# Optimization experiments

Measured on AMD Instinct MI355X. Metric: run time of the kernel, lower is better.

## Reference

```python
import jax, jax.numpy as jnp
import numpy as np

EMBED_DIM = 256
NUM_HEADS = 8
NB = 8          # number of scenes (batches)
LQ = 256        # queries per scene
LS = 4096       # source points per scene
LN_EPS = 1e-5


def setup_inputs() -> dict:
    key = jax.random.key(0)
    ks = jax.random.split(key, 8)
    d = EMBED_DIM
    n_q, n_s = NB * LQ, NB * LS
    w_scale = d ** -0.5  # xavier-ish
    return {
        "source": jax.random.normal(ks[0], (n_s, d), jnp.float32),
        "query": jax.random.normal(ks[1], (n_q, d), jnp.float32),
        "source_pe": 0.1 * jax.random.normal(ks[2], (n_s, d), jnp.float32),
        "query_pe": 0.1 * jax.random.normal(ks[3], (n_q, d), jnp.float32),
        "in_proj_w": w_scale * jax.random.normal(ks[4], (3 * d, d), jnp.float32),
        "in_proj_b": jnp.zeros((3 * d,), jnp.float32),
        "out_w": w_scale * jax.random.normal(ks[5], (d, d), jnp.float32),
        "out_b": jnp.zeros((d,), jnp.float32),
        "ln_w": jnp.ones((d,), jnp.float32),
        "ln_b": jnp.zeros((d,), jnp.float32),
        # sorted equal-size segments: token i belongs to scene i // L
        "source_batch": (jnp.arange(n_s, dtype=jnp.int32) // LS).astype(jnp.int32),
        "query_batch": (jnp.arange(n_q, dtype=jnp.int32) // LQ).astype(jnp.int32),
        "B": NB,
    }


def reference(source, query, source_pe, query_pe, in_proj_w, in_proj_b,
              out_w, out_b, ln_w, ln_b, source_batch, query_batch, B):
    d = source.shape[-1]
    H = NUM_HEADS
    hd = d // H
    Lq = query.shape[0] // B
    Ls = source.shape[0] // B

    # batch ids are sorted equal segments -> per-scene gather == reshape
    q_in = (query + query_pe).reshape(B, Lq, d)   # q with pos embed
    k_in = (source + source_pe).reshape(B, Ls, d) # k with pos embed
    v_in = source.reshape(B, Ls, d)               # v without pos embed

    Wq, Wk, Wv = jnp.split(in_proj_w, 3, axis=0)
    bq, bk, bv = jnp.split(in_proj_b, 3)

    q = (q_in @ Wq.T + bq).reshape(B, Lq, H, hd)
    k = (k_in @ Wk.T + bk).reshape(B, Ls, H, hd)
    v = (v_in @ Wv.T + bv).reshape(B, Ls, H, hd)

    scores = jnp.einsum('bqhd,bkhd->bhqk', q, k) * (hd ** -0.5)
    attn = jax.nn.softmax(scores, axis=-1)
    o = jnp.einsum('bhqk,bkhd->bqhd', attn, v).reshape(B, Lq, d)
    o = o @ out_w.T + out_b

    # residual (dropout is identity at p=0) + LayerNorm
    res = o + query.reshape(B, Lq, d)
    mu = jnp.mean(res, axis=-1, keepdims=True)
    var = jnp.var(res, axis=-1, keepdims=True)
    y = (res - mu) * jax.lax.rsqrt(var + LN_EPS) * ln_w + ln_b
    return y.reshape(-1, d)
```

## Files before the change

### kernel.cpp

```cpp
#include <hip/hip_runtime.h>
#include <hip/hip_bf16.h>

typedef __bf16 bf16;
typedef __bf16 bf16x4 __attribute__((ext_vector_type(4)));
typedef __bf16 bf16x8 __attribute__((ext_vector_type(8)));
typedef float f32x4 __attribute__((ext_vector_type(4)));

#define D 256
#define NHEAD 8
#define HD 32
#define NB_ 8
#define LQ_ 256
#define LS_ 4096
#define MQ (NB_ * LQ_)
#define MS (NB_ * LS_)

#define QSCALE 0.25500527f

__global__ __launch_bounds__(256) void prep(
    const float* __restrict__ source, const float* __restrict__ source_pe,
    const float* __restrict__ query, const float* __restrict__ query_pe,
    const float* __restrict__ w_in, const float* __restrict__ w_out,
    bf16* __restrict__ SPb, bf16* __restrict__ QPb, bf16* __restrict__ Wb)
{
    const int NS4 = MS * D / 4;
    const int NQ4 = MQ * D / 4;
    const int NW4 = (768 * 256 + 256 * 256) / 4;
    const int total = NS4 + NQ4 + NW4;
    for (int i = blockIdx.x * 256 + threadIdx.x; i < total; i += gridDim.x * 256) {
        if (i < NS4) {
            const float4 s = ((const float4*)source)[i];
            const float4 p = ((const float4*)source_pe)[i];
            bf16x4 osp;
            osp[0] = (bf16)(s.x + p.x); osp[1] = (bf16)(s.y + p.y);
            osp[2] = (bf16)(s.z + p.z); osp[3] = (bf16)(s.w + p.w);
            ((bf16x4*)SPb)[i] = osp;
        } else if (i < NS4 + NQ4) {
            const int j = i - NS4;
            const float4 s = ((const float4*)query)[j];
            const float4 p = ((const float4*)query_pe)[j];
            bf16x4 o;
            o[0] = (bf16)(s.x + p.x); o[1] = (bf16)(s.y + p.y);
            o[2] = (bf16)(s.z + p.z); o[3] = (bf16)(s.w + p.w);
            ((bf16x4*)QPb)[j] = o;
        } else {
            const int j = i - NS4 - NQ4;
            const float4 v = (j < 49152) ? ((const float4*)w_in)[j]
                                         : ((const float4*)w_out)[j - 49152];
            bf16x4 o;
            o[0] = (bf16)v.x; o[1] = (bf16)v.y; o[2] = (bf16)v.z; o[3] = (bf16)v.w;
            ((bf16x4*)Wb)[j] = o;
        }
    }
}

__global__ __launch_bounds__(256, 4) void gemm_proj(
    const bf16* __restrict__ SPb, const float* __restrict__ srcf,
    const bf16* __restrict__ QPb, const bf16* __restrict__ Wb,
    const float* __restrict__ in_proj_b,
    bf16* __restrict__ Kt, bf16* __restrict__ Vt2, bf16* __restrict__ Qb)
{
    __shared__ __align__(16) bf16 smem[2][128][72];
    bf16 (*As)[72] = smem[0];
    bf16 (*Bs)[72] = smem[1];
    const int tid = threadIdx.x, lane = tid & 63, wid = tid >> 6;
    const int wm = wid >> 1, wn = wid & 1;
    const int g = lane >> 4, q15 = lane & 15;
    const int id = blockIdx.x;

    const bf16* A; const bf16* W; const float* bias; bf16* out;
    int omode, mblk, nblk;
    if (id < 512) {
        A = SPb; W = Wb + 256 * D; bias = in_proj_b + 256; out = Kt;
        mblk = id >> 1; nblk = id & 1; omode = 1;
    } else if (id < 1024) {
        A = nullptr; W = Wb + 512 * D; bias = in_proj_b + 512; out = Vt2;
        mblk = (id - 512) >> 1; nblk = id & 1; omode = 2;
    } else {
        A = QPb; W = Wb; bias = in_proj_b; out = Qb;
        mblk = (id - 1024) >> 1; nblk = id & 1; omode = 0;
    }

    f32x4 acc[4][4];
    #pragma unroll
    for (int i = 0; i < 4; ++i)
        #pragma unroll
        for (int j = 0; j < 4; ++j) acc[i][j] = (f32x4){0.f, 0.f, 0.f, 0.f};

    const size_t arow0 = (size_t)mblk * 128;
    const int brow0 = nblk * 128;

    for (int kk = 0; kk < 4; ++kk) {
        const int d0 = kk * 64;
        if (omode == 2) {
            #pragma unroll
            for (int i = 0; i < 8; ++i) {
                const int idx = i * 256 + tid;
                const int r = idx >> 4, c = (idx & 15) * 4;
                const float4 v = *(const float4*)&srcf[(arow0 + r) * D + d0 + c];
                bf16x4 o;
                o[0] = (bf16)v.x; o[1] = (bf16)v.y; o[2] = (bf16)v.z; o[3] = (bf16)v.w;
                *(bf16x4*)&As[r][c] = o;
            }
            #pragma unroll
            for (int i = 0; i < 4; ++i) {
                const int idx = i * 256 + tid;
                const int r = idx >> 3, c = (idx & 7) * 8;
                *(bf16x8*)&Bs[r][c] = *(const bf16x8*)&W[(size_t)(brow0 + r) * D + d0 + c];
            }
        } else {
            #pragma unroll
            for (int i = 0; i < 4; ++i) {
                const int idx = i * 256 + tid;
                const int r = idx >> 3, c = (idx & 7) * 8;
                *(bf16x8*)&As[r][c] = *(const bf16x8*)&A[(arow0 + r) * D + d0 + c];
                *(bf16x8*)&Bs[r][c] = *(const bf16x8*)&W[(size_t)(brow0 + r) * D + d0 + c];
            }
        }
        __syncthreads();
        #pragma unroll
        for (int h2 = 0; h2 < 2; ++h2) {
            const int ko = h2 * 32 + g * 8;
            bf16x8 af[4], bfr[4];
            #pragma unroll
            for (int i = 0; i < 4; ++i)
                af[i] = *(const bf16x8*)&As[wm * 64 + i * 16 + q15][ko];
            #pragma unroll
            for (int j = 0; j < 4; ++j)
                bfr[j] = *(const bf16x8*)&Bs[wn * 64 + j * 16 + q15][ko];
            #pragma unroll
            for (int i = 0; i < 4; ++i)
                #pragma unroll
                for (int j = 0; j < 4; ++j)
                    acc[i][j] = __builtin_amdgcn_mfma_f32_16x16x32_bf16(
                        af[i], bfr[j], acc[i][j], 0, 0, 0);
        }
        __syncthreads();
    }

    if (omode == 0) {
        #pragma unroll
        for (int i = 0; i < 4; ++i)
            #pragma unroll
            for (int j = 0; j < 4; ++j) {
                const int n_g = nblk * 128 + wn * 64 + j * 16 + q15;
                const float b = bias[n_g];
                #pragma unroll
                for (int r = 0; r < 4; ++r) {
                    const size_t m_g = arow0 + wm * 64 + i * 16 + g * 4 + r;
                    out[m_g * D + n_g] = (bf16)((acc[i][j][r] + b) * QSCALE);
                }
            }
    } else if (omode == 1) {
        bf16* Ls = &smem[0][0][0];
        #pragma unroll
        for (int i = 0; i < 4; ++i)
            #pragma unroll
            for (int j = 0; j < 4; ++j) {
                const int n_loc = wn * 64 + j * 16 + q15;
                const int h_loc = n_loc >> 5, d = n_loc & 31;
                const int gp = d >> 3, e = d & 7;
                const float b = bias[nblk * 128 + n_loc];
                #pragma unroll
                for (int r = 0; r < 4; ++r) {
                    const int m_loc = wm * 64 + i * 16 + g * 4 + r;
                    const int c_loc = m_loc >> 6, kl = m_loc & 63;
                    const int t = ((kl >> 5) << 1) | ((kl >> 2) & 1);
                    const int q15p = ((kl >> 3) & 3) * 4 + (kl & 3);
                    Ls[(h_loc * 2 + c_loc) * 2048 + t * 512
                       + (gp * 16 + q15p) * 8 + e] = (bf16)(acc[i][j][r] + b);
                }
            }
        __syncthreads();
        const int bb = (int)(arow0 >> 12);
        const int c0 = (int)((arow0 & 4095) >> 6);
        const int h0 = (nblk * 128) >> 5;
        #pragma unroll
        for (int p = 0; p < 8; ++p) {
            const int idx = p * 2048 + tid * 8;
            const int blk = idx >> 11, within = idx & 2047;
            *(bf16x8*)&out[((size_t)(bb * 8 + h0 + (blk >> 1)) * 64
                            + c0 + (blk & 1)) * 2048 + within]
                = *(const bf16x8*)&Ls[idx];
        }
    } else {
        #pragma unroll
        for (int i = 0; i < 4; ++i)
            #pragma unroll
            for (int j = 0; j < 4; ++j) {
                const int n_g = nblk * 128 + wn * 64 + j * 16 + q15;
                const int h = n_g >> 5, d = n_g & 31;
                const int dt = d >> 4, q15p = d & 15;
                const float b = bias[n_g];
                const size_t m_g0 = arow0 + wm * 64 + i * 16 + g * 4;
                const int bb = (int)(m_g0 >> 12);
                const int c = (int)((m_g0 & 4095) >> 6);
                const int kl0 = (int)(m_g0 & 63);
                const int half = kl0 >> 5, gp = (kl0 >> 3) & 3, e0 = kl0 & 7;
                const int f = dt * 2 + half;
                bf16x4 o;
                #pragma unroll
                for (int r = 0; r < 4; ++r) o[r] = (bf16)(acc[i][j][r] + b);
                *(bf16x4*)&out[((size_t)(bb * 8 + h) * 64 + c) * 2048
                               + f * 512 + (gp * 16 + q15p) * 8 + e0] = o;
            }
    }
}

template<int S>
__global__ __launch_bounds__(256, 4) void attn_kernel(
    const bf16* __restrict__ Qb, const bf16* __restrict__ Kt,
    const bf16* __restrict__ Vt2,
    bf16* __restrict__ accp, float* __restrict__ lp)
{
    const int tid = threadIdx.x, lane = tid & 63, wid = tid >> 6;
    const int q15 = lane & 15, g = lane >> 4;
    const int bid = blockIdx.x;
    const int h = bid & 7;
    const int inner = bid >> 3;
    const int split = inner % S;
    const int tmp = inner / S;
    const int qt = tmp & 1;
    const int b = tmp >> 1;
    constexpr int CHUNKS = LS_ / S / 64;

    const int q0 = b * LQ_ + qt * 128 + wid * 32;
    const bf16x8 qfA = *(const bf16x8*)&Qb[(size_t)(q0 + q15) * D + h * HD + g * 8];
    const bf16x8 qfB = *(const bf16x8*)&Qb[(size_t)(q0 + 16 + q15) * D + h * HD + g * 8];

    const f32x4 minit = (f32x4){-8.f, -8.f, -8.f, -8.f};
    const size_t cbase = ((size_t)(b * 8 + h) * 64 + split * CHUNKS) * 2048;
    const bf16* kp = Kt + cbase + lane * 8;
    const bf16* vp = Vt2 + cbase + lane * 8;

    float lA = 0.f, lB = 0.f;
    f32x4 accA0 = (f32x4){0.f, 0.f, 0.f, 0.f};
    f32x4 accA1 = (f32x4){0.f, 0.f, 0.f, 0.f};
    f32x4 accB0 = (f32x4){0.f, 0.f, 0.f, 0.f};
    f32x4 accB1 = (f32x4){0.f, 0.f, 0.f, 0.f};

    for (int kc = 0; kc < CHUNKS; ++kc) {
        const size_t co = (size_t)kc * 2048;

        bf16x8 kf[4], vf[4];
        #pragma unroll
        for (int t = 0; t < 4; ++t) kf[t] = *(const bf16x8*)&kp[co + t * 512];
        #pragma unroll
        for (int f = 0; f < 4; ++f) vf[f] = *(const bf16x8*)&vp[co + f * 512];

        f32x4 sA[4], sB[4];
        #pragma unroll
        for (int t = 0; t < 4; ++t)
            sA[t] = __builtin_amdgcn_mfma_f32_16x16x32_bf16(kf[t], qfA, minit, 0, 0, 0);
        #pragma unroll
        for (int t = 0; t < 4; ++t)
            sB[t] = __builtin_amdgcn_mfma_f32_16x16x32_bf16(kf[t], qfB, minit, 0, 0, 0);

        bf16x8 paA0, paA1, paB0, paB1;
        #pragma unroll
        for (int r = 0; r < 4; ++r) {
            const float a0 = exp2f(sA[0][r]);
            const float a1 = exp2f(sA[1][r]);
            const float a2 = exp2f(sA[2][r]);
            const float a3 = exp2f(sA[3][r]);
            lA += (a0 + a1) + (a2 + a3);
            paA0[r] = (bf16)a0; paA0[4 + r] = (bf16)a1;
            paA1[r] = (bf16)a2; paA1[4 + r] = (bf16)a3;
            const float b0 = exp2f(sB[0][r]);
            const float b1 = exp2f(sB[1][r]);
            const float b2 = exp2f(sB[2][r]);
            const float b3 = exp2f(sB[3][r]);
            lB += (b0 + b1) + (b2 + b3);
            paB0[r] = (bf16)b0; paB0[4 + r] = (bf16)b1;
            paB1[r] = (bf16)b2; paB1[4 + r] = (bf16)b3;
        }

        accA0 = __builtin_amdgcn_mfma_f32_16x16x32_bf16(paA0, vf[0], accA0, 0, 0, 0);
        accA0 = __builtin_amdgcn_mfma_f32_16x16x32_bf16(paA1, vf[1], accA0, 0, 0, 0);
        accA1 = __builtin_amdgcn_mfma_f32_16x16x32_bf16(paA0, vf[2], accA1, 0, 0, 0);
        accA1 = __builtin_amdgcn_mfma_f32_16x16x32_bf16(paA1, vf[3], accA1, 0, 0, 0);
        accB0 = __builtin_amdgcn_mfma_f32_16x16x32_bf16(paB0, vf[0], accB0, 0, 0, 0);
        accB0 = __builtin_amdgcn_mfma_f32_16x16x32_bf16(paB1, vf[1], accB0, 0, 0, 0);
        accB1 = __builtin_amdgcn_mfma_f32_16x16x32_bf16(paB0, vf[2], accB1, 0, 0, 0);
        accB1 = __builtin_amdgcn_mfma_f32_16x16x32_bf16(paB1, vf[3], accB1, 0, 0, 0);
    }

    lA += __shfl_xor(lA, 16);
    lA += __shfl_xor(lA, 32);
    lB += __shfl_xor(lB, 16);
    lB += __shfl_xor(lB, 32);

    const int qg16 = qt * 8 + wid * 2;
    const int taskA = (b * 8 + h) * 16 + qg16;
    const size_t baseA = ((size_t)(taskA * S + split) * 64 + lane) * 8;
    const size_t baseB = ((size_t)((taskA + 1) * S + split) * 64 + lane) * 8;
    bf16x4 oA0, oA1, oB0, oB1;
    #pragma unroll
    for (int r = 0; r < 4; ++r) {
        oA0[r] = (bf16)accA0[r]; oA1[r] = (bf16)accA1[r];
        oB0[r] = (bf16)accB0[r]; oB1[r] = (bf16)accB1[r];
    }
    *(bf16x4*)&accp[baseA]     = oA0;
    *(bf16x4*)&accp[baseA + 4] = oA1;
    *(bf16x4*)&accp[baseB]     = oB0;
    *(bf16x4*)&accp[baseB + 4] = oB1;
    if (lane < 16) {
        lp[(taskA * S + split) * 16 + lane] = lA;
        lp[((taskA + 1) * S + split) * 16 + lane] = lB;
    }
}

template<int S>
__global__ __launch_bounds__(256) void attn_combine(
    const bf16* __restrict__ accp, const float* __restrict__ lp,
    bf16* __restrict__ Ob)
{
    const int tid = threadIdx.x, lane = tid & 63, wid = tid >> 6;
    const int task = blockIdx.x * 4 + wid;
    const int g = lane >> 4, q15 = lane & 15;

    f32x4 o0 = (f32x4){0.f, 0.f, 0.f, 0.f};
    f32x4 o1 = (f32x4){0.f, 0.f, 0.f, 0.f};
    float ll = 0.f;
    #pragma unroll
    for (int s = 0; s < S; ++s) {
        const size_t base = ((size_t)(task * S + s) * 64 + lane) * 8;
        const bf16x8 v = *(const bf16x8*)&accp[base];
        #pragma unroll
        for (int r = 0; r < 4; ++r) { o0[r] += (float)v[r]; o1[r] += (float)v[4 + r]; }
        if (lane < 16) ll += lp[(task * S + s) * 16 + lane];
    }

    const int b = task >> 7, h = (task >> 4) & 7, qg = task & 15;
    #pragma unroll
    for (int r = 0; r < 4; ++r) {
        const float inv = 1.f / __shfl(ll, g * 4 + r);
        const size_t row = (size_t)b * LQ_ + qg * 16 + g * 4 + r;
        Ob[row * D + h * HD + q15]      = (bf16)(o0[r] * inv);
        Ob[row * D + h * HD + 16 + q15] = (bf16)(o1[r] * inv);
    }
}

__global__ __launch_bounds__(256) void out_ln_kernel(
    const bf16* __restrict__ Ob, const bf16* __restrict__ Wout,
    const float* __restrict__ out_b, const float* __restrict__ query,
    const float* __restrict__ lnw, const float* __restrict__ lnb,
    float* __restrict__ out)
{
    __shared__ bf16 As[32][72];
    __shared__ bf16 Bs[256][72];
    __shared__ float red[2][32][2];
    const int tid = threadIdx.x, lane = tid & 63, wid = tid >> 6;
    const int wm = wid >> 1, wn = wid & 1;
    const int g = lane >> 4, q15 = lane & 15;
    const size_t row0 = (size_t)blockIdx.x * 32;

    f32x4 acc[8];
    #pragma unroll
    for (int j = 0; j < 8; ++j) acc[j] = (f32x4){0.f, 0.f, 0.f, 0.f};

    for (int kk = 0; kk < 4; ++kk) {
        const int d0 = kk * 64;
        {
            const int r = tid >> 3, c = (tid & 7) * 8;
            *(bf16x8*)&As[r][c] = *(const bf16x8*)&Ob[(row0 + r) * D + d0 + c];
        }
        #pragma unroll
        for (int i = 0; i < 8; ++i) {
            const int idx = i * 256 + tid;
            const int r = idx >> 3, c = (idx & 7) * 8;
            *(bf16x8*)&Bs[r][c] = *(const bf16x8*)&Wout[(size_t)r * D + d0 + c];
        }
        __syncthreads();
        #pragma unroll
        for (int h2 = 0; h2 < 2; ++h2) {
            const int ko = h2 * 32 + g * 8;
            const bf16x8 af = *(const bf16x8*)&As[wm * 16 + q15][ko];
            #pragma unroll
            for (int j = 0; j < 8; ++j) {
                const bf16x8 bfr = *(const bf16x8*)&Bs[wn * 128 + j * 16 + q15][ko];
                acc[j] = __builtin_amdgcn_mfma_f32_16x16x32_bf16(af, bfr, acc[j], 0, 0, 0);
            }
        }
        __syncthreads();
    }

    float bl[8], lw[8], lbv[8];
    #pragma unroll
    for (int j = 0; j < 8; ++j) {
        const int n = wn * 128 + j * 16 + q15;
        bl[j] = out_b[n]; lw[j] = lnw[n]; lbv[j] = lnb[n];
    }

    #pragma unroll
    for (int r = 0; r < 4; ++r) {
        const int rl = wm * 16 + g * 4 + r;
        const size_t m = row0 + rl;
        float s = 0.f, sq = 0.f;
        #pragma unroll
        for (int j = 0; j < 8; ++j) {
            const float v = acc[j][r] + bl[j] + query[m * D + wn * 128 + j * 16 + q15];
            acc[j][r] = v;
            s += v; sq += v * v;
        }
        s += __shfl_xor(s, 1);  sq += __shfl_xor(sq, 1);
        s += __shfl_xor(s, 2);  sq += __shfl_xor(sq, 2);
        s += __shfl_xor(s, 4);  sq += __shfl_xor(sq, 4);
        s += __shfl_xor(s, 8);  sq += __shfl_xor(sq, 8);
        if (q15 == r) {
            red[wn][rl][0] = s;
            red[wn][rl][1] = sq;
        }
    }
    __syncthreads();

    #pragma unroll
    for (int r = 0; r < 4; ++r) {
        const int rl = wm * 16 + g * 4 + r;
        const float s  = red[0][rl][0] + red[1][rl][0];
        const float sq = red[0][rl][1] + red[1][rl][1];
        const float mean = s * (1.f / 256.f);
        const float var  = sq * (1.f / 256.f) - mean * mean;
        const float inv  = rsqrtf(var + 1e-5f);
        const size_t m = row0 + rl;
        #pragma unroll
        for (int j = 0; j < 8; ++j)
            out[m * D + wn * 128 + j * 16 + q15] =
                (acc[j][r] - mean) * inv * lw[j] + lbv[j];
    }
}

extern "C" void kernel_launch(void* const* d_in, const int* in_sizes, int n_in,
                              void* d_out, int out_size, void* d_ws, size_t ws_size,
                              hipStream_t stream) {
    (void)in_sizes; (void)n_in; (void)out_size; (void)ws_size;
    const float* source    = (const float*)d_in[0];
    const float* query     = (const float*)d_in[1];
    const float* source_pe = (const float*)d_in[2];
    const float* query_pe  = (const float*)d_in[3];
    const float* in_proj_w = (const float*)d_in[4];
    const float* in_proj_b = (const float*)d_in[5];
    const float* out_w     = (const float*)d_in[6];
    const float* out_b     = (const float*)d_in[7];
    const float* ln_w      = (const float*)d_in[8];
    const float* ln_b      = (const float*)d_in[9];

    constexpr int S = 8;
    bf16* Wb   = (bf16*)d_ws;
    bf16* QPb  = Wb + 1024 * 256;
    bf16* Qb   = QPb + (size_t)MQ * D;
    bf16* Kt   = Qb + (size_t)MQ * D;
    bf16* Vt2  = Kt + (size_t)MS * D;
    bf16* SPb  = Vt2 + (size_t)MS * D;
    bf16* Ob   = SPb + (size_t)MS * D;
    bf16* accp = Ob + (size_t)MQ * D;
    float* lp  = (float*)(accp + (size_t)1024 * S * 64 * 8);
    float* outp = (float*)d_out;

    prep<<<dim3(2048), dim3(256), 0, stream>>>(
        source, source_pe, query, query_pe, in_proj_w, out_w,
        SPb, QPb, Wb);
    gemm_proj<<<dim3(1056), dim3(256), 0, stream>>>(
        SPb, source, QPb, Wb, in_proj_b, Kt, Vt2, Qb);
    attn_kernel<S><<<dim3(1024), dim3(256), 0, stream>>>(Qb, Kt, Vt2, accp, lp);
    attn_combine<S><<<dim3(256), dim3(256), 0, stream>>>(accp, lp, Ob);
    out_ln_kernel<<<dim3(64), dim3(256), 0, stream>>>(
        Ob, Wb + 768 * 256, out_b, query, ln_w, ln_b, outp);
}
```

Measured before the change: 81.01 us.

## Fuse pos-embed add into projection GEMM and split-K combine into out-proj LN

Removes the prep pass that materialized bf16 source+pe and query+pe buffers; the projection GEMM now loads fp32 inputs, adds the positional embedding and casts to bf16 while filling shared memory. A small kernel now only casts the weights. The separate attention combine kernel is folded into the output-projection/LayerNorm kernel, which reduces the split partials straight into a full-row shared tile, so the Ob buffer is no longer written or read. This cuts global traffic and launches, at the cost of the K-projection blocks reading two fp32 arrays, and the out-proj kernel running only 64 blocks, which now also do the combine work.

```diff
diff --git a/kernel.cpp b/kernel.cpp
--- a/kernel.cpp
+++ b/kernel.cpp
@@ -17,47 +17,24 @@
 
 #define QSCALE 0.25500527f
 
-__global__ __launch_bounds__(256) void prep(
+__global__ __launch_bounds__(256) void wcast(
+    const float* __restrict__ w_in, const float* __restrict__ w_out,
+    bf16* __restrict__ wb)
+{
+    const int idx = blockIdx.x * 256 + threadIdx.x;
+    const int n_in4 = (768 * 256) / 4;
+    float4 v;
+    if (idx < n_in4) v = ((const float4*)w_in)[idx];
+    else             v = ((const float4*)w_out)[idx - n_in4];
+    bf16x4 o;
+    o[0] = (bf16)v.x; o[1] = (bf16)v.y; o[2] = (bf16)v.z; o[3] = (bf16)v.w;
+    *(bf16x4*)&wb[(size_t)idx * 4] = o;
+}
+
+__global__ __launch_bounds__(256, 4) void gemm_proj(
     const float* __restrict__ source, const float* __restrict__ source_pe,
     const float* __restrict__ query, const float* __restrict__ query_pe,
-    const float* __restrict__ w_in, const float* __restrict__ w_out,
-    bf16* __restrict__ SPb, bf16* __restrict__ QPb, bf16* __restrict__ Wb)
-{
-    const int NS4 = MS * D / 4;
-    const int NQ4 = MQ * D / 4;
-    const int NW4 = (768 * 256 + 256 * 256) / 4;
-    const int total = NS4 + NQ4 + NW4;
-    for (int i = blockIdx.x * 256 + threadIdx.x; i < total; i += gridDim.x * 256) {
-        if (i < NS4) {
-            const float4 s = ((const float4*)source)[i];
-            const float4 p = ((const float4*)source_pe)[i];
-            bf16x4 osp;
-            osp[0] = (bf16)(s.x + p.x); osp[1] = (bf16)(s.y + p.y);
-            osp[2] = (bf16)(s.z + p.z); osp[3] = (bf16)(s.w + p.w);
-            ((bf16x4*)SPb)[i] = osp;
-        } else if (i < NS4 + NQ4) {
-            const int j = i - NS4;
-            const float4 s = ((const float4*)query)[j];
-            const float4 p = ((const float4*)query_pe)[j];
-            bf16x4 o;
-            o[0] = (bf16)(s.x + p.x); o[1] = (bf16)(s.y + p.y);
-            o[2] = (bf16)(s.z + p.z); o[3] = (bf16)(s.w + p.w);
-            ((bf16x4*)QPb)[j] = o;
-        } else {
-            const int j = i - NS4 - NQ4;
-            const float4 v = (j < 49152) ? ((const float4*)w_in)[j]
-                                         : ((const float4*)w_out)[j - 49152];
-            bf16x4 o;
-            o[0] = (bf16)v.x; o[1] = (bf16)v.y; o[2] = (bf16)v.z; o[3] = (bf16)v.w;
-            ((bf16x4*)Wb)[j] = o;
-        }
-    }
-}
-
-__global__ __launch_bounds__(256, 4) void gemm_proj(
-    const bf16* __restrict__ SPb, const float* __restrict__ srcf,
-    const bf16* __restrict__ QPb, const bf16* __restrict__ Wb,
-    const float* __restrict__ in_proj_b,
+    const bf16* __restrict__ Wb, const float* __restrict__ in_proj_b,
     bf16* __restrict__ Kt, bf16* __restrict__ Vt2, bf16* __restrict__ Qb)
 {
     __shared__ __align__(16) bf16 smem[2][128][72];
@@ -68,17 +45,17 @@
     const int g = lane >> 4, q15 = lane & 15;
     const int id = blockIdx.x;
 
-    const bf16* A; const bf16* W; const float* bias; bf16* out;
+    const float* A; const float* P; const bf16* W; const float* bias; bf16* out;
     int omode, mblk, nblk;
     if (id < 512) {
-        A = SPb; W = Wb + 256 * D; bias = in_proj_b + 256; out = Kt;
-        mblk = id >> 1; nblk = id & 1; omode = 1;
+        A = source; P = source_pe; W = Wb + 256 * D; bias = in_proj_b + 256;
+        out = Kt; mblk = id >> 1; nblk = id & 1; omode = 1;
     } else if (id < 1024) {
-        A = nullptr; W = Wb + 512 * D; bias = in_proj_b + 512; out = Vt2;
-        mblk = (id - 512) >> 1; nblk = id & 1; omode = 2;
+        A = source; P = nullptr; W = Wb + 512 * D; bias = in_proj_b + 512;
+        out = Vt2; mblk = (id - 512) >> 1; nblk = id & 1; omode = 2;
     } else {
-        A = QPb; W = Wb; bias = in_proj_b; out = Qb;
-        mblk = (id - 1024) >> 1; nblk = id & 1; omode = 0;
+        A = query; P = query_pe; W = Wb; bias = in_proj_b;
+        out = Qb; mblk = (id - 1024) >> 1; nblk = id & 1; omode = 0;
     }
 
     f32x4 acc[4][4];
@@ -92,30 +69,25 @@
 
     for (int kk = 0; kk < 4; ++kk) {
         const int d0 = kk * 64;
-        if (omode == 2) {
-            #pragma unroll
-            for (int i = 0; i < 8; ++i) {
-                const int idx = i * 256 + tid;
-                const int r = idx >> 4, c = (idx & 15) * 4;
-                const float4 v = *(const float4*)&srcf[(arow0 + r) * D + d0 + c];
-                bf16x4 o;
-                o[0] = (bf16)v.x; o[1] = (bf16)v.y; o[2] = (bf16)v.z; o[3] = (bf16)v.w;
-                *(bf16x4*)&As[r][c] = o;
+        #pragma unroll
+        for (int i = 0; i < 8; ++i) {
+            const int idx = i * 256 + tid;
+            const int r = idx >> 4, c = (idx & 15) * 4;
+            const size_t gof = (arow0 + r) * D + d0 + c;
+            float4 v = *(const float4*)&A[gof];
+            if (P) {
+                const float4 p = *(const float4*)&P[gof];
+                v.x += p.x; v.y += p.y; v.z += p.z; v.w += p.w;
             }
-            #pragma unroll
-            for (int i = 0; i < 4; ++i) {
-                const int idx = i * 256 + tid;
-                const int r = idx >> 3, c = (idx & 7) * 8;
-                *(bf16x8*)&Bs[r][c] = *(const bf16x8*)&W[(size_t)(brow0 + r) * D + d0 + c];
-            }
-        } else {
-            #pragma unroll
-            for (int i = 0; i < 4; ++i) {
-                const int idx = i * 256 + tid;
-                const int r = idx >> 3, c = (idx & 7) * 8;
-                *(bf16x8*)&As[r][c] = *(const bf16x8*)&A[(arow0 + r) * D + d0 + c];
-                *(bf16x8*)&Bs[r][c] = *(const bf16x8*)&W[(size_t)(brow0 + r) * D + d0 + c];
-            }
+            bf16x4 o;
+            o[0] = (bf16)v.x; o[1] = (bf16)v.y; o[2] = (bf16)v.z; o[3] = (bf16)v.w;
+            *(bf16x4*)&As[r][c] = o;
+        }
+        #pragma unroll
+        for (int i = 0; i < 4; ++i) {
+            const int idx = i * 256 + tid;
+            const int r = idx >> 3, c = (idx & 7) * 8;
+            *(bf16x8*)&Bs[r][c] = *(const bf16x8*)&W[(size_t)(brow0 + r) * D + d0 + c];
         }
         __syncthreads();
         #pragma unroll
@@ -311,49 +283,48 @@
 }
 
 template<int S>
-__global__ __launch_bounds__(256) void attn_combine(
+__global__ __launch_bounds__(256) void out_ln_kernel(
     const bf16* __restrict__ accp, const float* __restrict__ lp,
-    bf16* __restrict__ Ob)
-{
-    const int tid = threadIdx.x, lane = tid & 63, wid = tid >> 6;
-    const int task = blockIdx.x * 4 + wid;
-    const int g = lane >> 4, q15 = lane & 15;
-
-    f32x4 o0 = (f32x4){0.f, 0.f, 0.f, 0.f};
-    f32x4 o1 = (f32x4){0.f, 0.f, 0.f, 0.f};
-    float ll = 0.f;
-    #pragma unroll
-    for (int s = 0; s < S; ++s) {
-        const size_t base = ((size_t)(task * S + s) * 64 + lane) * 8;
-        const bf16x8 v = *(const bf16x8*)&accp[base];
-        #pragma unroll
-        for (int r = 0; r < 4; ++r) { o0[r] += (float)v[r]; o1[r] += (float)v[4 + r]; }
-        if (lane < 16) ll += lp[(task * S + s) * 16 + lane];
-    }
-
-    const int b = task >> 7, h = (task >> 4) & 7, qg = task & 15;
-    #pragma unroll
-    for (int r = 0; r < 4; ++r) {
-        const float inv = 1.f / __shfl(ll, g * 4 + r);
-        const size_t row = (size_t)b * LQ_ + qg * 16 + g * 4 + r;
-        Ob[row * D + h * HD + q15]      = (bf16)(o0[r] * inv);
-        Ob[row * D + h * HD + 16 + q15] = (bf16)(o1[r] * inv);
-    }
-}
-
-__global__ __launch_bounds__(256) void out_ln_kernel(
-    const bf16* __restrict__ Ob, const bf16* __restrict__ Wout,
+    const bf16* __restrict__ Wout,
     const float* __restrict__ out_b, const float* __restrict__ query,
     const float* __restrict__ lnw, const float* __restrict__ lnb,
     float* __restrict__ out)
 {
-    __shared__ bf16 As[32][72];
+    __shared__ bf16 As2[32][288];
     __shared__ bf16 Bs[256][72];
     __shared__ float red[2][32][2];
     const int tid = threadIdx.x, lane = tid & 63, wid = tid >> 6;
     const int wm = wid >> 1, wn = wid & 1;
     const int g = lane >> 4, q15 = lane & 15;
     const size_t row0 = (size_t)blockIdx.x * 32;
+    const int b = (int)(row0 >> 8);
+    const int qg0 = (int)((row0 & 255) >> 4);
+
+    #pragma unroll
+    for (int k = 0; k < 4; ++k) {
+        const int t = wid * 4 + k;
+        const int h = t >> 1, dq = t & 1;
+        const int task = (b * 8 + h) * 16 + qg0 + dq;
+        f32x4 o0 = (f32x4){0.f, 0.f, 0.f, 0.f};
+        f32x4 o1 = (f32x4){0.f, 0.f, 0.f, 0.f};
+        float ll = 0.f;
+        #pragma unroll
+        for (int s = 0; s < S; ++s) {
+            const size_t base = ((size_t)(task * S + s) * 64 + lane) * 8;
+            const bf16x8 v = *(const bf16x8*)&accp[base];
+            #pragma unroll
+            for (int r = 0; r < 4; ++r) { o0[r] += (float)v[r]; o1[r] += (float)v[4 + r]; }
+            if (lane < 16) ll += lp[(task * S + s) * 16 + lane];
+        }
+        #pragma unroll
+        for (int r = 0; r < 4; ++r) {
+            const float inv = 1.f / __shfl(ll, g * 4 + r);
+            const int rl = dq * 16 + g * 4 + r;
+            As2[rl][h * 32 + q15]      = (bf16)(o0[r] * inv);
+            As2[rl][h * 32 + 16 + q15] = (bf16)(o1[r] * inv);
+        }
+    }
+    __syncthreads();
 
     f32x4 acc[8];
     #pragma unroll
@@ -361,10 +332,6 @@
 
     for (int kk = 0; kk < 4; ++kk) {
         const int d0 = kk * 64;
-        {
-            const int r = tid >> 3, c = (tid & 7) * 8;
-            *(bf16x8*)&As[r][c] = *(const bf16x8*)&Ob[(row0 + r) * D + d0 + c];
-        }
         #pragma unroll
         for (int i = 0; i < 8; ++i) {
             const int idx = i * 256 + tid;
@@ -375,7 +342,7 @@
         #pragma unroll
         for (int h2 = 0; h2 < 2; ++h2) {
             const int ko = h2 * 32 + g * 8;
-            const bf16x8 af = *(const bf16x8*)&As[wm * 16 + q15][ko];
+            const bf16x8 af = *(const bf16x8*)&As2[wm * 16 + q15][d0 + ko];
             #pragma unroll
             for (int j = 0; j < 8; ++j) {
                 const bf16x8 bfr = *(const bf16x8*)&Bs[wn * 128 + j * 16 + q15][ko];
@@ -447,23 +414,17 @@
 
     constexpr int S = 8;
     bf16* Wb   = (bf16*)d_ws;
-    bf16* QPb  = Wb + 1024 * 256;
-    bf16* Qb   = QPb + (size_t)MQ * D;
+    bf16* Qb   = Wb + 1024 * 256;
     bf16* Kt   = Qb + (size_t)MQ * D;
     bf16* Vt2  = Kt + (size_t)MS * D;
-    bf16* SPb  = Vt2 + (size_t)MS * D;
-    bf16* Ob   = SPb + (size_t)MS * D;
-    bf16* accp = Ob + (size_t)MQ * D;
+    bf16* accp = Vt2 + (size_t)MS * D;
     float* lp  = (float*)(accp + (size_t)1024 * S * 64 * 8);
     float* outp = (float*)d_out;
 
-    prep<<<dim3(2048), dim3(256), 0, stream>>>(
-        source, source_pe, query, query_pe, in_proj_w, out_w,
-        SPb, QPb, Wb);
+    wcast<<<dim3(256), dim3(256), 0, stream>>>(in_proj_w, out_w, Wb);
     gemm_proj<<<dim3(1056), dim3(256), 0, stream>>>(
-        SPb, source, QPb, Wb, in_proj_b, Kt, Vt2, Qb);
+        source, source_pe, query, query_pe, Wb, in_proj_b, Kt, Vt2, Qb);
     attn_kernel<S><<<dim3(1024), dim3(256), 0, stream>>>(Qb, Kt, Vt2, accp, lp);
-    attn_combine<S><<<dim3(256), dim3(256), 0, stream>>>(accp, lp, Ob);
-    out_ln_kernel<<<dim3(64), dim3(256), 0, stream>>>(
-        Ob, Wb + 768 * 256, out_b, query, ln_w, ln_b, outp);
+    out_ln_kernel<S><<<dim3(64), dim3(256), 0, stream>>>(
+        accp, lp, Wb + 768 * 256, out_b, query, ln_w, ln_b, outp);
 }
```

New measurement: 113.4 us. 40.0% more time.

## Process 64 queries per wave in attention to halve K/V reloads

Applied to the files above, without the earlier changes.

Each wave now handles four 16-query fragments (64 queries) instead of two, so a block covers all 256 queries of a scene and each K/V chunk loaded from global memory is reused across twice as many queries. The grid halves to 512 blocks and the occupancy hint drops from 4 to 2 blocks per CU to make room for the extra accumulator registers. The cost is lower occupancy and fewer blocks, which may expose load latency more.

```diff
diff --git a/kernel.cpp b/kernel.cpp
--- a/kernel.cpp
+++ b/kernel.cpp
@@ -208,7 +208,7 @@
 }
 
 template<int S>
-__global__ __launch_bounds__(256, 4) void attn_kernel(
+__global__ __launch_bounds__(256, 2) void attn_kernel(
     const bf16* __restrict__ Qb, const bf16* __restrict__ Kt,
     const bf16* __restrict__ Vt2,
     bf16* __restrict__ accp, float* __restrict__ lp)
@@ -219,25 +219,27 @@
     const int h = bid & 7;
     const int inner = bid >> 3;
     const int split = inner % S;
-    const int tmp = inner / S;
-    const int qt = tmp & 1;
-    const int b = tmp >> 1;
+    const int b = inner / S;
     constexpr int CHUNKS = LS_ / S / 64;
 
-    const int q0 = b * LQ_ + qt * 128 + wid * 32;
-    const bf16x8 qfA = *(const bf16x8*)&Qb[(size_t)(q0 + q15) * D + h * HD + g * 8];
-    const bf16x8 qfB = *(const bf16x8*)&Qb[(size_t)(q0 + 16 + q15) * D + h * HD + g * 8];
+    const int q0 = b * LQ_ + wid * 64;
+    bf16x8 qf[4];
+    #pragma unroll
+    for (int f = 0; f < 4; ++f)
+        qf[f] = *(const bf16x8*)&Qb[(size_t)(q0 + f * 16 + q15) * D + h * HD + g * 8];
 
     const f32x4 minit = (f32x4){-8.f, -8.f, -8.f, -8.f};
     const size_t cbase = ((size_t)(b * 8 + h) * 64 + split * CHUNKS) * 2048;
     const bf16* kp = Kt + cbase + lane * 8;
     const bf16* vp = Vt2 + cbase + lane * 8;
 
-    float lA = 0.f, lB = 0.f;
-    f32x4 accA0 = (f32x4){0.f, 0.f, 0.f, 0.f};
-    f32x4 accA1 = (f32x4){0.f, 0.f, 0.f, 0.f};
-    f32x4 accB0 = (f32x4){0.f, 0.f, 0.f, 0.f};
-    f32x4 accB1 = (f32x4){0.f, 0.f, 0.f, 0.f};
+    float lr[4] = {0.f, 0.f, 0.f, 0.f};
+    f32x4 a0[4], a1[4];
+    #pragma unroll
+    for (int f = 0; f < 4; ++f) {
+        a0[f] = (f32x4){0.f, 0.f, 0.f, 0.f};
+        a1[f] = (f32x4){0.f, 0.f, 0.f, 0.f};
+    }
 
     for (int kc = 0; kc < CHUNKS; ++kc) {
         const size_t co = (size_t)kc * 2048;
@@ -246,67 +248,52 @@
         #pragma unroll
         for (int t = 0; t < 4; ++t) kf[t] = *(const bf16x8*)&kp[co + t * 512];
         #pragma unroll
-        for (int f = 0; f < 4; ++f) vf[f] = *(const bf16x8*)&vp[co + f * 512];
-
-        f32x4 sA[4], sB[4];
-        #pragma unroll
-        for (int t = 0; t < 4; ++t)
-            sA[t] = __builtin_amdgcn_mfma_f32_16x16x32_bf16(kf[t], qfA, minit, 0, 0, 0);
-        #pragma unroll
-        for (int t = 0; t < 4; ++t)
-            sB[t] = __builtin_amdgcn_mfma_f32_16x16x32_bf16(kf[t], qfB, minit, 0, 0, 0);
-
-        bf16x8 paA0, paA1, paB0, paB1;
+        for (int t = 0; t < 4; ++t) vf[t] = *(const bf16x8*)&vp[co + t * 512];
+
+        #pragma unroll
+        for (int f = 0; f < 4; ++f) {
+            f32x4 s0 = __builtin_amdgcn_mfma_f32_16x16x32_bf16(kf[0], qf[f], minit, 0, 0, 0);
+            f32x4 s1 = __builtin_amdgcn_mfma_f32_16x16x32_bf16(kf[1], qf[f], minit, 0, 0, 0);
+            f32x4 s2 = __builtin_amdgcn_mfma_f32_16x16x32_bf16(kf[2], qf[f], minit, 0, 0, 0);
+            f32x4 s3 = __builtin_amdgcn_mfma_f32_16x16x32_bf16(kf[3], qf[f], minit, 0, 0, 0);
+
+            bf16x8 pa0, pa1;
+            #pragma unroll
+            for (int r = 0; r < 4; ++r) {
+                const float p0 = exp2f(s0[r]);
+                const float p1 = exp2f(s1[r]);
+                const float p2 = exp2f(s2[r]);
+                const float p3 = exp2f(s3[r]);
+                lr[f] += (p0 + p1) + (p2 + p3);
+                pa0[r]     = (bf16)p0;
+                pa0[4 + r] = (bf16)p1;
+                pa1[r]     = (bf16)p2;
+                pa1[4 + r] = (bf16)p3;
+            }
+
+            a0[f] = __builtin_amdgcn_mfma_f32_16x16x32_bf16(pa0, vf[0], a0[f], 0, 0, 0);
+            a0[f] = __builtin_amdgcn_mfma_f32_16x16x32_bf16(pa1, vf[1], a0[f], 0, 0, 0);
+            a1[f] = __builtin_amdgcn_mfma_f32_16x16x32_bf16(pa0, vf[2], a1[f], 0, 0, 0);
+            a1[f] = __builtin_amdgcn_mfma_f32_16x16x32_bf16(pa1, vf[3], a1[f], 0, 0, 0);
+        }
+    }
+
+    const int task0 = (b * 8 + h) * 16 + wid * 4;
+    #pragma unroll
+    for (int f = 0; f < 4; ++f) {
+        lr[f] += __shfl_xor(lr[f], 16);
+        lr[f] += __shfl_xor(lr[f], 32);
+        const size_t base = ((size_t)((task0 + f) * S + split) * 64 + lane) * 8;
+        bf16x4 o0, o1;
         #pragma unroll
         for (int r = 0; r < 4; ++r) {
-            const float a0 = exp2f(sA[0][r]);
-            const float a1 = exp2f(sA[1][r]);
-            const float a2 = exp2f(sA[2][r]);
-            const float a3 = exp2f(sA[3][r]);
-            lA += (a0 + a1) + (a2 + a3);
-            paA0[r] = (bf16)a0; paA0[4 + r] = (bf16)a1;
-            paA1[r] = (bf16)a2; paA1[4 + r] = (bf16)a3;
-            const float b0 = exp2f(sB[0][r]);
-            const float b1 = exp2f(sB[1][r]);
-            const float b2 = exp2f(sB[2][r]);
-            const float b3 = exp2f(sB[3][r]);
-            lB += (b0 + b1) + (b2 + b3);
-            paB0[r] = (bf16)b0; paB0[4 + r] = (bf16)b1;
-            paB1[r] = (bf16)b2; paB1[4 + r] = (bf16)b3;
-        }
-
-        accA0 = __builtin_amdgcn_mfma_f32_16x16x32_bf16(paA0, vf[0], accA0, 0, 0, 0);
-        accA0 = __builtin_amdgcn_mfma_f32_16x16x32_bf16(paA1, vf[1], accA0, 0, 0, 0);
-        accA1 = __builtin_amdgcn_mfma_f32_16x16x32_bf16(paA0, vf[2], accA1, 0, 0, 0);
-        accA1 = __builtin_amdgcn_mfma_f32_16x16x32_bf16(paA1, vf[3], accA1, 0, 0, 0);
-        accB0 = __builtin_amdgcn_mfma_f32_16x16x32_bf16(paB0, vf[0], accB0, 0, 0, 0);
-        accB0 = __builtin_amdgcn_mfma_f32_16x16x32_bf16(paB1, vf[1], accB0, 0, 0, 0);
-        accB1 = __builtin_amdgcn_mfma_f32_16x16x32_bf16(paB0, vf[2], accB1, 0, 0, 0);
-        accB1 = __builtin_amdgcn_mfma_f32_16x16x32_bf16(paB1, vf[3], accB1, 0, 0, 0);
-    }
-
-    lA += __shfl_xor(lA, 16);
-    lA += __shfl_xor(lA, 32);
-    lB += __shfl_xor(lB, 16);
-    lB += __shfl_xor(lB, 32);
-
-    const int qg16 = qt * 8 + wid * 2;
-    const int taskA = (b * 8 + h) * 16 + qg16;
-    const size_t baseA = ((size_t)(taskA * S + split) * 64 + lane) * 8;
-    const size_t baseB = ((size_t)((taskA + 1) * S + split) * 64 + lane) * 8;
-    bf16x4 oA0, oA1, oB0, oB1;
-    #pragma unroll
-    for (int r = 0; r < 4; ++r) {
-        oA0[r] = (bf16)accA0[r]; oA1[r] = (bf16)accA1[r];
-        oB0[r] = (bf16)accB0[r]; oB1[r] = (bf16)accB1[r];
-    }
-    *(bf16x4*)&accp[baseA]     = oA0;
-    *(bf16x4*)&accp[baseA + 4] = oA1;
-    *(bf16x4*)&accp[baseB]     = oB0;
-    *(bf16x4*)&accp[baseB + 4] = oB1;
-    if (lane < 16) {
-        lp[(taskA * S + split) * 16 + lane] = lA;
-        lp[((taskA + 1) * S + split) * 16 + lane] = lB;
+            o0[r] = (bf16)a0[f][r];
+            o1[r] = (bf16)a1[f][r];
+        }
+        *(bf16x4*)&accp[base]     = o0;
+        *(bf16x4*)&accp[base + 4] = o1;
+        if (lane < 16)
+            lp[((task0 + f) * S + split) * 16 + lane] = lr[f];
     }
 }
 
@@ -462,7 +449,7 @@
         SPb, QPb, Wb);
     gemm_proj<<<dim3(1056), dim3(256), 0, stream>>>(
         SPb, source, QPb, Wb, in_proj_b, Kt, Vt2, Qb);
-    attn_kernel<S><<<dim3(1024), dim3(256), 0, stream>>>(Qb, Kt, Vt2, accp, lp);
+    attn_kernel<S><<<dim3(512), dim3(256), 0, stream>>>(Qb, Kt, Vt2, accp, lp);
     attn_combine<S><<<dim3(256), dim3(256), 0, stream>>>(accp, lp, Ob);
     out_ln_kernel<<<dim3(64), dim3(256), 0, stream>>>(
         Ob, Wb + 768 * 256, out_b, query, ln_w, ln_b, outp);
```

Measured after the change: 82.27 us. About the same (+1.5%).
